# Optimization experiments

Hardware: AMD Instinct MI355X
Metric: run time of the kernel (lower is better)

## Reference

```python
import jax, jax.numpy as jnp
import numpy as np


def setup_inputs() -> dict:
    key = jax.random.key(0)
    k1, k2, k3, k4 = jax.random.split(key, 4)
    B, idf, cdf, h, w, L = 32, 256, 256, 64, 64, 128
    x = jax.random.normal(k1, (B, idf, h, w), dtype=jnp.float32)
    context = jax.random.normal(k2, (B, cdf, L), dtype=jnp.float32)
    # conv1x1 weight (no bias): [idf, cdf]
    W = jax.random.normal(k3, (idf, cdf), dtype=jnp.float32) / np.sqrt(cdf)
    mask = jax.random.randint(k4, (B, L), 0, 2).astype(bool)
    return {"x": x, "context": context, "W": W, "mask": mask}


def reference(x, context, W, mask):
    B, idf, h, w = x.shape
    hxw = h * w
    L = context.shape[2]
    # conv1x1 projection of context: [B, idf, L]
    source = jnp.einsum('ic,bcl->bil', W, context)
    target = x.reshape(B, idf, hxw)
    # QK^T: [B, hxw, L]
    attn = jnp.einsum('bip,bil->bpl', target, source)
    # faithful to torch: mask [B, L] is tiled hxw times over the flattened
    # [B*hxw, L] view (row order b*hxw+p vs tile order p*B+b, as in original)
    attn_flat = attn.reshape(B * hxw, L)
    attn_flat = jnp.where(jnp.tile(mask, (hxw, 1)), -jnp.inf, attn_flat)
    attn = jax.nn.softmax(attn_flat, axis=-1).reshape(B, hxw, L)
    attn_t = jnp.swapaxes(attn, 1, 2)  # [B, L, hxw]
    # PV: [B, idf, hxw] -> [B, idf, h, w]
    result = jnp.einsum('bil,blp->bip', source, attn_t).reshape(B, idf, h, w)
    return result, attn_t.reshape(B, L, h, w)
```

## Files before the change

kernel.cpp:

```cpp
#include <hip/hip_runtime.h>
#include <cstdint>

#define IDF 256
#define CDF 256
#define NL  128
#define HXW 4096
#define NB  32
#define PTILE 64

typedef _Float16 f16x8 __attribute__((ext_vector_type(8)));
typedef __fp16 fp16x2 __attribute__((ext_vector_type(2)));
typedef float f32x4 __attribute__((ext_vector_type(4)));
typedef unsigned short u16;
typedef unsigned int u32;

union Frag { f16x8 v; u32 u[4]; uint2 u2[2]; uint4 u4; };

__device__ __forceinline__ u16 f2h(float f) { union { _Float16 h; u16 s; } c; c.h = (_Float16)f; return c.s; }
__device__ __forceinline__ u32 pkrtz(float a, float b) {
  union { fp16x2 v; u32 u; } c;
  c.v = __builtin_amdgcn_cvt_pkrtz(a, b);
  return c.u;
}


__global__ __launch_bounds__(256) void proj_kernel(const float* __restrict__ W,
                                                   const float* __restrict__ ctx,
                                                   u16* __restrict__ srcF,
                                                   u16* __restrict__ srcT,
                                                   const u32* __restrict__ msk,
                                                   u32* __restrict__ ws0) {
  const int tid = threadIdx.x;
  if (blockIdx.x == 0 && blockIdx.y == 0) {
    __shared__ int bi_s, bf_s, mode_s;
    if (tid == 0) { bi_s = 0; bf_s = 0; }
    __syncthreads();
    int bi = 0, bfl = 0;
    for (int k = 0; k < 4; ++k) {
      u32 v = msk[tid * 4 + k];
      if (v > 1u) bi = 1;
      float f = __uint_as_float(v);
      if (!(f == 0.0f || f == 1.0f)) bfl = 1;
    }
    if (bi) atomicOr(&bi_s, 1);
    if (bfl) atomicOr(&bf_s, 1);
    __syncthreads();
    if (tid == 0) { mode_s = (bi_s == 0) ? 0 : ((bf_s == 0) ? 1 : 2); ws0[0] = (u32)mode_s; }
    __syncthreads();
    const int mode = mode_s;
    if (tid < 128) {
      int row = tid >> 2, q = tid & 3;
      u32 bits = 0;
      for (int c = 0; c < 32; ++c) {
        int idx = row * NL + q * 32 + c;
        int mv;
        if (mode == 0)      mv = ((const int*)msk)[idx] != 0;
        else if (mode == 1) mv = ((const float*)msk)[idx] != 0.0f;
        else                mv = ((const unsigned char*)msk)[idx] != 0;
        bits |= (u32)mv << c;
      }
      ws0[64 + row * 4 + q] = bits;
    }
  }

  __shared__ float sWt[16][33];
  __shared__ float sC[16 * NL];
  const int b = blockIdx.y;
  const int i0 = blockIdx.x * 32;
  const int tx = tid & 31;
  const int ty = tid >> 5;
  float acc[4][4] = {};
  const float* ctxb = ctx + (size_t)b * CDF * NL;
  for (int c0 = 0; c0 < CDF; c0 += 16) {
    if (tid < 128) {
      int i = tid >> 2, cq = tid & 3;
      float4 w4 = *(const float4*)(W + (size_t)(i0 + i) * CDF + c0 + cq * 4);
      sWt[cq * 4 + 0][i] = w4.x; sWt[cq * 4 + 1][i] = w4.y;
      sWt[cq * 4 + 2][i] = w4.z; sWt[cq * 4 + 3][i] = w4.w;
    }
#pragma unroll
    for (int k = 0; k < 2; ++k) {
      int idx = tid + k * 256;
      int r = idx >> 5, c4 = idx & 31;
      *(float4*)(sC + r * NL + c4 * 4) =
          *(const float4*)(ctxb + (size_t)(c0 + r) * NL + c4 * 4);
    }
    __syncthreads();
#pragma unroll
    for (int cc = 0; cc < 16; ++cc) {
      float4 c4 = *(const float4*)(sC + cc * NL + tx * 4);
#pragma unroll
      for (int ii = 0; ii < 4; ++ii) {
        float w = sWt[cc][ty * 4 + ii];
        acc[ii][0] = fmaf(w, c4.x, acc[ii][0]);
        acc[ii][1] = fmaf(w, c4.y, acc[ii][1]);
        acc[ii][2] = fmaf(w, c4.z, acc[ii][2]);
        acc[ii][3] = fmaf(w, c4.w, acc[ii][3]);
      }
    }
    __syncthreads();
  }
  u16* sf = srcF + (size_t)b * IDF * NL;
  u16* st = srcT + (size_t)b * NL * IDF;
#pragma unroll
  for (int ii = 0; ii < 4; ++ii) {
    int i = i0 + ty * 4 + ii;
    u32 d0 = pkrtz(acc[ii][0], acc[ii][1]);
    u32 d1 = pkrtz(acc[ii][2], acc[ii][3]);
    *(uint2*)(sf + (size_t)i * NL + tx * 4) = make_uint2(d0, d1);
#pragma unroll
    for (int jl = 0; jl < 4; ++jl)
      st[(size_t)(tx * 4 + jl) * IDF + i] = f2h(acc[ii][jl]);
  }
}

__global__ __launch_bounds__(256, 4) void attn_kernel(
    const float* __restrict__ x, const u16* __restrict__ srcF,
    const u16* __restrict__ srcT, const u32* __restrict__ wsm,
    float* __restrict__ out0, float* __restrict__ out1) {
  __shared__ __align__(16) u32 sBuf[128 * 66];

  const int tid = threadIdx.x;
  const int lane = tid & 63;
  const int w = tid >> 6;
  const int m15 = lane & 15;
  const int g = lane >> 4;
  const int b = blockIdx.y;
  const int p0 = blockIdx.x * PTILE;
  const int pl = w * 16 + m15;

  {
    const float* xb = x + (size_t)b * IDF * HXW + p0;
    const int t16 = tid >> 4;
    const int p4 = (tid & 15) * 4;
    float4 lo[8], hi[8];
#pragma unroll
    for (int it = 0; it < 8; ++it) {
      const float* rp = xb + (size_t)(it * 32 + t16 * 2) * HXW + p4;
      lo[it] = *(const float4*)rp;
      hi[it] = *(const float4*)(rp + HXW);
    }
#pragma unroll
    for (int it = 0; it < 8; ++it) {
      int base = (it * 16 + t16) * 66 + p4;
      u32 r0 = pkrtz(lo[it].x, hi[it].x);
      u32 r1 = pkrtz(lo[it].y, hi[it].y);
      u32 r2 = pkrtz(lo[it].z, hi[it].z);
      u32 r3 = pkrtz(lo[it].w, hi[it].w);
      *(uint2*)(sBuf + base + 0) = make_uint2(r0, r1);
      *(uint2*)(sBuf + base + 2) = make_uint2(r2, r3);
    }
  }
  __syncthreads();

  f32x4 accq[8];
#pragma unroll
  for (int nt = 0; nt < 8; ++nt) accq[nt] = f32x4{0.f, 0.f, 0.f, 0.f};

  const u16* stb = srcT + (size_t)b * NL * IDF;
#pragma unroll
  for (int ic = 0; ic < 8; ++ic) {
    Frag bf[8];
#pragma unroll
    for (int nt = 0; nt < 8; ++nt)
      bf[nt].u4 = *(const uint4*)(stb + (size_t)(nt * 16 + m15) * IDF + ic * 32 + g * 8);
    Frag bx;
#pragma unroll
    for (int jj = 0; jj < 4; ++jj)
      bx.u[jj] = sBuf[(ic * 16 + g * 4 + jj) * 66 + pl];
#pragma unroll
    for (int nt = 0; nt < 8; ++nt)
      accq[nt] = __builtin_amdgcn_mfma_f32_16x16x32_f16(bf[nt].v, bx.v, accq[nt], 0, 0, 0);
  }

  const int rm = pl & 31;
  uint4 mr = *(const uint4*)(wsm + rm * 4);
  u32 mw[4] = {mr.x, mr.y, mr.z, mr.w};
  float mx = -3.0e38f;
#pragma unroll
  for (int nt = 0; nt < 8; ++nt) {
    u32 bits = mw[nt >> 1] >> ((nt & 1) * 16);
#pragma unroll
    for (int r = 0; r < 4; ++r) {
      if ((bits >> (g * 4 + r)) & 1u) accq[nt][r] = -3.0e38f;
      mx = fmaxf(mx, accq[nt][r]);
    }
  }
  mx = fmaxf(mx, __shfl_xor(mx, 16));
  mx = fmaxf(mx, __shfl_xor(mx, 32));
  float s = 0.f;
#pragma unroll
  for (int nt = 0; nt < 8; ++nt)
#pragma unroll
    for (int r = 0; r < 4; ++r) {
      float e = __expf(accq[nt][r] - mx);
      accq[nt][r] = e;
      s += e;
    }
  s += __shfl_xor(s, 16);
  s += __shfl_xor(s, 32);
  const float inv = 1.0f / s;

  float* o1 = out1 + (size_t)b * NL * HXW + p0 + pl;
#pragma unroll
  for (int nt = 0; nt < 8; ++nt)
#pragma unroll
    for (int r = 0; r < 4; ++r) {
      float v = accq[nt][r] * inv;
      accq[nt][r] = v;
      o1[(size_t)(nt * 16 + g * 4 + r) * HXW] = v;
    }
  __syncthreads();
#pragma unroll
  for (int nt = 0; nt < 8; ++nt) {
    sBuf[pl * 66 + nt * 8 + g * 2 + 0] = pkrtz(accq[nt][0], accq[nt][1]);
    sBuf[pl * 66 + nt * 8 + g * 2 + 1] = pkrtz(accq[nt][2], accq[nt][3]);
  }
  __syncthreads();

  f32x4 accp[4][4];
#pragma unroll
  for (int mt = 0; mt < 4; ++mt)
#pragma unroll
    for (int nt2 = 0; nt2 < 4; ++nt2) accp[mt][nt2] = f32x4{0.f, 0.f, 0.f, 0.f};

  const u16* sfb = srcF + (size_t)b * IDF * NL;
#pragma unroll
  for (int ks = 0; ks < 4; ++ks) {
    Frag af[4], bf[4];
#pragma unroll
    for (int mt = 0; mt < 4; ++mt)
      af[mt].u4 = *(const uint4*)(sfb + (size_t)(w * 64 + mt * 16 + m15) * NL + ks * 32 + g * 8);
#pragma unroll
    for (int nt2 = 0; nt2 < 4; ++nt2) {
      int di = (nt2 * 16 + m15) * 66 + ks * 16 + g * 4;
      bf[nt2].u2[0] = *(const uint2*)(sBuf + di);
      bf[nt2].u2[1] = *(const uint2*)(sBuf + di + 2);
    }
#pragma unroll
    for (int mt = 0; mt < 4; ++mt)
#pragma unroll
      for (int nt2 = 0; nt2 < 4; ++nt2)
        accp[mt][nt2] = __builtin_amdgcn_mfma_f32_16x16x32_f16(af[mt].v, bf[nt2].v, accp[mt][nt2], 0, 0, 0);
  }

  float* o0 = out0 + (size_t)b * IDF * HXW + p0;
#pragma unroll
  for (int mt = 0; mt < 4; ++mt)
#pragma unroll
    for (int nt2 = 0; nt2 < 4; ++nt2) {
      int col = nt2 * 16 + m15;
#pragma unroll
      for (int r = 0; r < 4; ++r) {
        int row = w * 64 + mt * 16 + g * 4 + r;
        o0[(size_t)row * HXW + col] = accp[mt][nt2][r];
      }
    }
}

extern "C" void kernel_launch(void* const* d_in, const int* in_sizes, int n_in,
                              void* d_out, int out_size, void* d_ws, size_t ws_size,
                              hipStream_t stream) {
  const float* x   = (const float*)d_in[0];
  const float* ctx = (const float*)d_in[1];
  const float* W   = (const float*)d_in[2];
  const void*  msk = d_in[3];
  float* out0 = (float*)d_out;
  float* out1 = out0 + (size_t)NB * IDF * HXW;
  u32* ws0 = (u32*)d_ws;
  u16* srcF = (u16*)((char*)d_ws + 1024);
  u16* srcT = (u16*)((char*)d_ws + 1024 + 2097152);

  proj_kernel<<<dim3(8, NB), 256, 0, stream>>>(W, ctx, srcF, srcT, (const u32*)msk, ws0);
  attn_kernel<<<dim3(HXW / PTILE, NB), 256, 0, stream>>>(x, srcF, srcT, ws0 + 64, out0, out1);
}
```

Measured before the change: 151.2 us.

## Halve pixel tile, split softmax over waves, double-buffer fragment loads

Shrinks the per-block pixel tile from 64 to 32, which doubles the grid. Each pair of waves now handles half of the L dimension and merges the partial softmax max and sum through a small shared-memory exchange. Global fragment loads for the QK and PV matmuls are double-buffered so the next chunk is fetched while MFMAs run. This aims for more parallelism and better latency hiding, at the cost of rereading the projected source per pixel twice as often and an extra barrier.

```diff
diff --git a/kernel.cpp b/kernel.cpp
--- a/kernel.cpp
+++ b/kernel.cpp
@@ -6,7 +6,7 @@
 #define NL  128
 #define HXW 4096
 #define NB  32
-#define PTILE 64
+#define PTILE 32
 
 typedef _Float16 f16x8 __attribute__((ext_vector_type(8)));
 typedef __fp16 fp16x2 __attribute__((ext_vector_type(2)));
@@ -118,68 +118,81 @@
     const float* __restrict__ x, const u16* __restrict__ srcF,
     const u16* __restrict__ srcT, const u32* __restrict__ wsm,
     float* __restrict__ out0, float* __restrict__ out1) {
-  __shared__ __align__(16) u32 sBuf[128 * 66];
+  __shared__ __align__(16) u32 sBuf[128 * 35];
+  __shared__ float2 sM[2][32];
 
   const int tid = threadIdx.x;
   const int lane = tid & 63;
   const int w = tid >> 6;
   const int m15 = lane & 15;
   const int g = lane >> 4;
+  const int half = w >> 1;
+  const int wq = w & 1;
   const int b = blockIdx.y;
   const int p0 = blockIdx.x * PTILE;
-  const int pl = w * 16 + m15;
-
-  {
-    const float* xb = x + (size_t)b * IDF * HXW + p0;
-    const int t16 = tid >> 4;
-    const int p4 = (tid & 15) * 4;
-    float4 lo[8], hi[8];
-#pragma unroll
-    for (int it = 0; it < 8; ++it) {
-      const float* rp = xb + (size_t)(it * 32 + t16 * 2) * HXW + p4;
-      lo[it] = *(const float4*)rp;
-      hi[it] = *(const float4*)(rp + HXW);
-    }
-#pragma unroll
-    for (int it = 0; it < 8; ++it) {
-      int base = (it * 16 + t16) * 66 + p4;
-      u32 r0 = pkrtz(lo[it].x, hi[it].x);
-      u32 r1 = pkrtz(lo[it].y, hi[it].y);
-      u32 r2 = pkrtz(lo[it].z, hi[it].z);
-      u32 r3 = pkrtz(lo[it].w, hi[it].w);
-      *(uint2*)(sBuf + base + 0) = make_uint2(r0, r1);
-      *(uint2*)(sBuf + base + 2) = make_uint2(r2, r3);
-    }
+  const int pl = wq * 16 + m15;
+
+  const u16* stb = srcT + (size_t)b * NL * IDF;
+
+  const float* xb = x + (size_t)b * IDF * HXW + p0;
+  const int kq = tid >> 3;
+  const int p4 = (tid & 7) * 4;
+  float4 lo[4], hi[4];
+#pragma unroll
+  for (int it = 0; it < 4; ++it) {
+    const float* rp = xb + (size_t)(it * 64 + kq * 2) * HXW + p4;
+    lo[it] = *(const float4*)rp;
+    hi[it] = *(const float4*)(rp + HXW);
+  }
+
+  Frag bufA[4], bufB[4];
+#define LOAD_ST(dst, ic_)                                                              \
+  {                                                                                    \
+    _Pragma("unroll")                                                                  \
+    for (int nt = 0; nt < 4; ++nt)                                                     \
+      dst[nt].u4 = *(const uint4*)(stb + (size_t)((half * 4 + nt) * 16 + m15) * IDF +  \
+                                   (ic_) * 32 + g * 8);                                \
+  }
+  LOAD_ST(bufA, 0)
+
+#pragma unroll
+  for (int it = 0; it < 4; ++it) {
+    int base = (it * 32 + kq) * 35 + p4;
+    sBuf[base + 0] = pkrtz(lo[it].x, hi[it].x);
+    sBuf[base + 1] = pkrtz(lo[it].y, hi[it].y);
+    sBuf[base + 2] = pkrtz(lo[it].z, hi[it].z);
+    sBuf[base + 3] = pkrtz(lo[it].w, hi[it].w);
   }
   __syncthreads();
 
-  f32x4 accq[8];
-#pragma unroll
-  for (int nt = 0; nt < 8; ++nt) accq[nt] = f32x4{0.f, 0.f, 0.f, 0.f};
-
-  const u16* stb = srcT + (size_t)b * NL * IDF;
+  f32x4 accq[4];
+#pragma unroll
+  for (int nt = 0; nt < 4; ++nt) accq[nt] = f32x4{0.f, 0.f, 0.f, 0.f};
+
 #pragma unroll
   for (int ic = 0; ic < 8; ++ic) {
-    Frag bf[8];
-#pragma unroll
-    for (int nt = 0; nt < 8; ++nt)
-      bf[nt].u4 = *(const uint4*)(stb + (size_t)(nt * 16 + m15) * IDF + ic * 32 + g * 8);
+    if (ic < 7) {
+      if (ic & 1) { LOAD_ST(bufA, ic + 1) } else { LOAD_ST(bufB, ic + 1) }
+    }
     Frag bx;
 #pragma unroll
     for (int jj = 0; jj < 4; ++jj)
-      bx.u[jj] = sBuf[(ic * 16 + g * 4 + jj) * 66 + pl];
-#pragma unroll
-    for (int nt = 0; nt < 8; ++nt)
-      accq[nt] = __builtin_amdgcn_mfma_f32_16x16x32_f16(bf[nt].v, bx.v, accq[nt], 0, 0, 0);
+      bx.u[jj] = sBuf[(ic * 16 + g * 4 + jj) * 35 + pl];
+#pragma unroll
+    for (int nt = 0; nt < 4; ++nt) {
+      const Frag& af = (ic & 1) ? bufB[nt] : bufA[nt];
+      accq[nt] = __builtin_amdgcn_mfma_f32_16x16x32_f16(af.v, bx.v, accq[nt], 0, 0, 0);
+    }
   }
 
   const int rm = pl & 31;
   uint4 mr = *(const uint4*)(wsm + rm * 4);
-  u32 mw[4] = {mr.x, mr.y, mr.z, mr.w};
+  u32 mwv[4] = {mr.x, mr.y, mr.z, mr.w};
   float mx = -3.0e38f;
 #pragma unroll
-  for (int nt = 0; nt < 8; ++nt) {
-    u32 bits = mw[nt >> 1] >> ((nt & 1) * 16);
+  for (int nt = 0; nt < 4; ++nt) {
+    int lt = half * 4 + nt;
+    u32 bits = mwv[lt >> 1] >> ((lt & 1) * 16);
 #pragma unroll
     for (int r = 0; r < 4; ++r) {
       if ((bits >> (g * 4 + r)) & 1u) accq[nt][r] = -3.0e38f;
@@ -190,7 +203,7 @@
   mx = fmaxf(mx, __shfl_xor(mx, 32));
   float s = 0.f;
 #pragma unroll
-  for (int nt = 0; nt < 8; ++nt)
+  for (int nt = 0; nt < 4; ++nt)
 #pragma unroll
     for (int r = 0; r < 4; ++r) {
       float e = __expf(accq[nt][r] - mx);
@@ -199,61 +212,79 @@
     }
   s += __shfl_xor(s, 16);
   s += __shfl_xor(s, 32);
-  const float inv = 1.0f / s;
+  if (g == 0) sM[half][pl] = make_float2(mx, s);
+  __syncthreads();
+  float2 o = sM[half ^ 1][pl];
+  float m = fmaxf(mx, o.x);
+  float f = __expf(mx - m);
+  float s_tot = s * f + o.y * __expf(o.x - m);
+  const float inv = f / s_tot;
+
+  u32* sAd = sBuf;
+#pragma unroll
+  for (int nt = 0; nt < 4; ++nt) {
+#pragma unroll
+    for (int r = 0; r < 4; ++r) accq[nt][r] *= inv;
+    sAd[pl * 66 + (half * 4 + nt) * 8 + g * 2 + 0] = pkrtz(accq[nt][0], accq[nt][1]);
+    sAd[pl * 66 + (half * 4 + nt) * 8 + g * 2 + 1] = pkrtz(accq[nt][2], accq[nt][3]);
+  }
+  __syncthreads();
+
+  const u16* sfb = srcF + (size_t)b * IDF * NL;
+  Frag afA[4], afB[4];
+#define LOAD_SF(dst, ks_)                                                              \
+  {                                                                                    \
+    _Pragma("unroll")                                                                  \
+    for (int mt = 0; mt < 4; ++mt)                                                     \
+      dst[mt].u4 = *(const uint4*)(sfb + (size_t)(w * 64 + mt * 16 + m15) * NL +       \
+                                   (ks_) * 32 + g * 8);                                \
+  }
+  LOAD_SF(afA, 0)
 
   float* o1 = out1 + (size_t)b * NL * HXW + p0 + pl;
 #pragma unroll
-  for (int nt = 0; nt < 8; ++nt)
-#pragma unroll
-    for (int r = 0; r < 4; ++r) {
-      float v = accq[nt][r] * inv;
-      accq[nt][r] = v;
-      o1[(size_t)(nt * 16 + g * 4 + r) * HXW] = v;
-    }
-  __syncthreads();
-#pragma unroll
-  for (int nt = 0; nt < 8; ++nt) {
-    sBuf[pl * 66 + nt * 8 + g * 2 + 0] = pkrtz(accq[nt][0], accq[nt][1]);
-    sBuf[pl * 66 + nt * 8 + g * 2 + 1] = pkrtz(accq[nt][2], accq[nt][3]);
-  }
-  __syncthreads();
-
-  f32x4 accp[4][4];
+  for (int nt = 0; nt < 4; ++nt)
+#pragma unroll
+    for (int r = 0; r < 4; ++r)
+      o1[(size_t)((half * 4 + nt) * 16 + g * 4 + r) * HXW] = accq[nt][r];
+
+  f32x4 accp[4][2];
 #pragma unroll
   for (int mt = 0; mt < 4; ++mt)
 #pragma unroll
-    for (int nt2 = 0; nt2 < 4; ++nt2) accp[mt][nt2] = f32x4{0.f, 0.f, 0.f, 0.f};
-
-  const u16* sfb = srcF + (size_t)b * IDF * NL;
+    for (int n2 = 0; n2 < 2; ++n2) accp[mt][n2] = f32x4{0.f, 0.f, 0.f, 0.f};
+
 #pragma unroll
   for (int ks = 0; ks < 4; ++ks) {
-    Frag af[4], bf[4];
-#pragma unroll
-    for (int mt = 0; mt < 4; ++mt)
-      af[mt].u4 = *(const uint4*)(sfb + (size_t)(w * 64 + mt * 16 + m15) * NL + ks * 32 + g * 8);
-#pragma unroll
-    for (int nt2 = 0; nt2 < 4; ++nt2) {
-      int di = (nt2 * 16 + m15) * 66 + ks * 16 + g * 4;
-      bf[nt2].u2[0] = *(const uint2*)(sBuf + di);
-      bf[nt2].u2[1] = *(const uint2*)(sBuf + di + 2);
-    }
-#pragma unroll
-    for (int mt = 0; mt < 4; ++mt)
-#pragma unroll
-      for (int nt2 = 0; nt2 < 4; ++nt2)
-        accp[mt][nt2] = __builtin_amdgcn_mfma_f32_16x16x32_f16(af[mt].v, bf[nt2].v, accp[mt][nt2], 0, 0, 0);
+    if (ks < 3) {
+      if (ks & 1) { LOAD_SF(afA, ks + 1) } else { LOAD_SF(afB, ks + 1) }
+    }
+    Frag bf[2];
+#pragma unroll
+    for (int n2 = 0; n2 < 2; ++n2) {
+      int di = (n2 * 16 + m15) * 66 + ks * 16 + g * 4;
+      bf[n2].u2[0] = *(const uint2*)(sAd + di);
+      bf[n2].u2[1] = *(const uint2*)(sAd + di + 2);
+    }
+#pragma unroll
+    for (int mt = 0; mt < 4; ++mt) {
+      const Frag& af = (ks & 1) ? afB[mt] : afA[mt];
+#pragma unroll
+      for (int n2 = 0; n2 < 2; ++n2)
+        accp[mt][n2] = __builtin_amdgcn_mfma_f32_16x16x32_f16(af.v, bf[n2].v, accp[mt][n2], 0, 0, 0);
+    }
   }
 
   float* o0 = out0 + (size_t)b * IDF * HXW + p0;
 #pragma unroll
   for (int mt = 0; mt < 4; ++mt)
 #pragma unroll
-    for (int nt2 = 0; nt2 < 4; ++nt2) {
-      int col = nt2 * 16 + m15;
+    for (int n2 = 0; n2 < 2; ++n2) {
+      int col = n2 * 16 + m15;
 #pragma unroll
       for (int r = 0; r < 4; ++r) {
         int row = w * 64 + mt * 16 + g * 4 + r;
-        o0[(size_t)row * HXW + col] = accp[mt][nt2][r];
+        o0[(size_t)row * HXW + col] = accp[mt][n2][r];
       }
     }
 }
```

Measured after the change: 181.4 us. 20.0% more time.

## Process two pixel tiles per block and prefetch next x tile during PV

Applied to the files above, without the earlier changes.

Each attention block now handles two consecutive 64-pixel tiles of the same batch, which halves the grid and moves the mask load and base pointers out of the per-tile work. The global loads of x for the second tile are issued during the last k-step of the first tile's PV MFMA loop, so that load latency overlaps compute. The launch bound no longer requests 4 blocks per SM, and holding the prefetched x registers (lo/hi) during the MFMA loop raises register pressure, which may reduce occupancy. The attention output store is also moved after the LDS writes.

```diff
diff --git a/kernel.cpp b/kernel.cpp
--- a/kernel.cpp
+++ b/kernel.cpp
@@ -114,7 +114,7 @@
   }
 }
 
-__global__ __launch_bounds__(256, 4) void attn_kernel(
+__global__ __launch_bounds__(256) void attn_kernel(
     const float* __restrict__ x, const u16* __restrict__ srcF,
     const u16* __restrict__ srcT, const u32* __restrict__ wsm,
     float* __restrict__ out0, float* __restrict__ out1) {
@@ -125,21 +125,41 @@
   const int w = tid >> 6;
   const int m15 = lane & 15;
   const int g = lane >> 4;
-  const int b = blockIdx.y;
-  const int p0 = blockIdx.x * PTILE;
+  const int bid = blockIdx.x;
+  const int tile0 = bid * 2;
+  const int b = tile0 >> 6;
   const int pl = w * 16 + m15;
 
-  {
-    const float* xb = x + (size_t)b * IDF * HXW + p0;
-    const int t16 = tid >> 4;
-    const int p4 = (tid & 15) * 4;
-    float4 lo[8], hi[8];
-#pragma unroll
-    for (int it = 0; it < 8; ++it) {
-      const float* rp = xb + (size_t)(it * 32 + t16 * 2) * HXW + p4;
-      lo[it] = *(const float4*)rp;
-      hi[it] = *(const float4*)(rp + HXW);
-    }
+  const u16* stb = srcT + (size_t)b * NL * IDF;
+  const u16* sfb = srcF + (size_t)b * IDF * NL;
+  const float* xbb = x + (size_t)b * IDF * HXW;
+
+  const int t16 = tid >> 4;
+  const int p4 = (tid & 15) * 4;
+
+  const int rm = pl & 31;
+  uint4 mr = *(const uint4*)(wsm + rm * 4);
+  u32 mwv[4] = {mr.x, mr.y, mr.z, mr.w};
+
+  float4 lo[8], hi[8];
+#define ISSUE_X(p0_)                                                          \
+  {                                                                           \
+    const float* xb = xbb + (p0_);                                            \
+    _Pragma("unroll")                                                         \
+    for (int it = 0; it < 8; ++it) {                                          \
+      const float* rp = xb + (size_t)(it * 32 + t16 * 2) * HXW + p4;          \
+      lo[it] = *(const float4*)rp;                                            \
+      hi[it] = *(const float4*)(rp + HXW);                                    \
+    }                                                                         \
+  }
+
+  ISSUE_X((tile0 & 63) * 64)
+
+#pragma unroll
+  for (int t = 0; t < 2; ++t) {
+    const int p0 = ((tile0 + t) & 63) * 64;
+    __syncthreads();
+
 #pragma unroll
     for (int it = 0; it < 8; ++it) {
       int base = (it * 16 + t16) * 66 + p4;
@@ -150,112 +170,110 @@
       *(uint2*)(sBuf + base + 0) = make_uint2(r0, r1);
       *(uint2*)(sBuf + base + 2) = make_uint2(r2, r3);
     }
-  }
-  __syncthreads();
-
-  f32x4 accq[8];
-#pragma unroll
-  for (int nt = 0; nt < 8; ++nt) accq[nt] = f32x4{0.f, 0.f, 0.f, 0.f};
-
-  const u16* stb = srcT + (size_t)b * NL * IDF;
-#pragma unroll
-  for (int ic = 0; ic < 8; ++ic) {
-    Frag bf[8];
+    __syncthreads();
+
+    f32x4 accq[8];
+#pragma unroll
+    for (int nt = 0; nt < 8; ++nt) accq[nt] = f32x4{0.f, 0.f, 0.f, 0.f};
+#pragma unroll
+    for (int ic = 0; ic < 8; ++ic) {
+      Frag bf[8];
+#pragma unroll
+      for (int nt = 0; nt < 8; ++nt)
+        bf[nt].u4 = *(const uint4*)(stb + (size_t)(nt * 16 + m15) * IDF + ic * 32 + g * 8);
+      Frag bx;
+#pragma unroll
+      for (int jj = 0; jj < 4; ++jj)
+        bx.u[jj] = sBuf[(ic * 16 + g * 4 + jj) * 66 + pl];
+#pragma unroll
+      for (int nt = 0; nt < 8; ++nt)
+        accq[nt] = __builtin_amdgcn_mfma_f32_16x16x32_f16(bf[nt].v, bx.v, accq[nt], 0, 0, 0);
+    }
+
+    float mx = -3.0e38f;
+#pragma unroll
+    for (int nt = 0; nt < 8; ++nt) {
+      u32 bits = mwv[nt >> 1] >> ((nt & 1) * 16);
+#pragma unroll
+      for (int r = 0; r < 4; ++r) {
+        if ((bits >> (g * 4 + r)) & 1u) accq[nt][r] = -3.0e38f;
+        mx = fmaxf(mx, accq[nt][r]);
+      }
+    }
+    mx = fmaxf(mx, __shfl_xor(mx, 16));
+    mx = fmaxf(mx, __shfl_xor(mx, 32));
+    float s = 0.f;
 #pragma unroll
     for (int nt = 0; nt < 8; ++nt)
-      bf[nt].u4 = *(const uint4*)(stb + (size_t)(nt * 16 + m15) * IDF + ic * 32 + g * 8);
-    Frag bx;
-#pragma unroll
-    for (int jj = 0; jj < 4; ++jj)
-      bx.u[jj] = sBuf[(ic * 16 + g * 4 + jj) * 66 + pl];
+#pragma unroll
+      for (int r = 0; r < 4; ++r) {
+        float e = __expf(accq[nt][r] - mx);
+        accq[nt][r] = e;
+        s += e;
+      }
+    s += __shfl_xor(s, 16);
+    s += __shfl_xor(s, 32);
+    const float inv = 1.0f / s;
 #pragma unroll
     for (int nt = 0; nt < 8; ++nt)
-      accq[nt] = __builtin_amdgcn_mfma_f32_16x16x32_f16(bf[nt].v, bx.v, accq[nt], 0, 0, 0);
-  }
-
-  const int rm = pl & 31;
-  uint4 mr = *(const uint4*)(wsm + rm * 4);
-  u32 mw[4] = {mr.x, mr.y, mr.z, mr.w};
-  float mx = -3.0e38f;
-#pragma unroll
-  for (int nt = 0; nt < 8; ++nt) {
-    u32 bits = mw[nt >> 1] >> ((nt & 1) * 16);
-#pragma unroll
-    for (int r = 0; r < 4; ++r) {
-      if ((bits >> (g * 4 + r)) & 1u) accq[nt][r] = -3.0e38f;
-      mx = fmaxf(mx, accq[nt][r]);
-    }
-  }
-  mx = fmaxf(mx, __shfl_xor(mx, 16));
-  mx = fmaxf(mx, __shfl_xor(mx, 32));
-  float s = 0.f;
-#pragma unroll
-  for (int nt = 0; nt < 8; ++nt)
-#pragma unroll
-    for (int r = 0; r < 4; ++r) {
-      float e = __expf(accq[nt][r] - mx);
-      accq[nt][r] = e;
-      s += e;
-    }
-  s += __shfl_xor(s, 16);
-  s += __shfl_xor(s, 32);
-  const float inv = 1.0f / s;
-
-  float* o1 = out1 + (size_t)b * NL * HXW + p0 + pl;
-#pragma unroll
-  for (int nt = 0; nt < 8; ++nt)
-#pragma unroll
-    for (int r = 0; r < 4; ++r) {
-      float v = accq[nt][r] * inv;
-      accq[nt][r] = v;
-      o1[(size_t)(nt * 16 + g * 4 + r) * HXW] = v;
-    }
-  __syncthreads();
-#pragma unroll
-  for (int nt = 0; nt < 8; ++nt) {
-    sBuf[pl * 66 + nt * 8 + g * 2 + 0] = pkrtz(accq[nt][0], accq[nt][1]);
-    sBuf[pl * 66 + nt * 8 + g * 2 + 1] = pkrtz(accq[nt][2], accq[nt][3]);
-  }
-  __syncthreads();
-
-  f32x4 accp[4][4];
-#pragma unroll
-  for (int mt = 0; mt < 4; ++mt)
-#pragma unroll
-    for (int nt2 = 0; nt2 < 4; ++nt2) accp[mt][nt2] = f32x4{0.f, 0.f, 0.f, 0.f};
-
-  const u16* sfb = srcF + (size_t)b * IDF * NL;
-#pragma unroll
-  for (int ks = 0; ks < 4; ++ks) {
-    Frag af[4], bf[4];
+#pragma unroll
+      for (int r = 0; r < 4; ++r) accq[nt][r] *= inv;
+
+    __syncthreads();
+
+#pragma unroll
+    for (int nt = 0; nt < 8; ++nt) {
+      sBuf[pl * 66 + nt * 8 + g * 2 + 0] = pkrtz(accq[nt][0], accq[nt][1]);
+      sBuf[pl * 66 + nt * 8 + g * 2 + 1] = pkrtz(accq[nt][2], accq[nt][3]);
+    }
+    float* o1 = out1 + (size_t)b * NL * HXW + p0 + pl;
+#pragma unroll
+    for (int nt = 0; nt < 8; ++nt)
+#pragma unroll
+      for (int r = 0; r < 4; ++r)
+        o1[(size_t)(nt * 16 + g * 4 + r) * HXW] = accq[nt][r];
+    __syncthreads();
+
+    f32x4 accp[4][4];
 #pragma unroll
     for (int mt = 0; mt < 4; ++mt)
-      af[mt].u4 = *(const uint4*)(sfb + (size_t)(w * 64 + mt * 16 + m15) * NL + ks * 32 + g * 8);
-#pragma unroll
-    for (int nt2 = 0; nt2 < 4; ++nt2) {
-      int di = (nt2 * 16 + m15) * 66 + ks * 16 + g * 4;
-      bf[nt2].u2[0] = *(const uint2*)(sBuf + di);
-      bf[nt2].u2[1] = *(const uint2*)(sBuf + di + 2);
-    }
+#pragma unroll
+      for (int nt2 = 0; nt2 < 4; ++nt2) accp[mt][nt2] = f32x4{0.f, 0.f, 0.f, 0.f};
+
+#pragma unroll
+    for (int ks = 0; ks < 4; ++ks) {
+      Frag af[4], bf[4];
+#pragma unroll
+      for (int mt = 0; mt < 4; ++mt)
+        af[mt].u4 = *(const uint4*)(sfb + (size_t)(w * 64 + mt * 16 + m15) * NL + ks * 32 + g * 8);
+      if (ks == 3 && t == 0)
+        ISSUE_X(((tile0 + 1) & 63) * 64)
+#pragma unroll
+      for (int nt2 = 0; nt2 < 4; ++nt2) {
+        int di = (nt2 * 16 + m15) * 66 + ks * 16 + g * 4;
+        bf[nt2].u2[0] = *(const uint2*)(sBuf + di);
+        bf[nt2].u2[1] = *(const uint2*)(sBuf + di + 2);
+      }
+#pragma unroll
+      for (int mt = 0; mt < 4; ++mt)
+#pragma unroll
+        for (int nt2 = 0; nt2 < 4; ++nt2)
+          accp[mt][nt2] = __builtin_amdgcn_mfma_f32_16x16x32_f16(af[mt].v, bf[nt2].v, accp[mt][nt2], 0, 0, 0);
+    }
+
+    float* o0 = out0 + (size_t)b * IDF * HXW + p0;
 #pragma unroll
     for (int mt = 0; mt < 4; ++mt)
 #pragma unroll
-      for (int nt2 = 0; nt2 < 4; ++nt2)
-        accp[mt][nt2] = __builtin_amdgcn_mfma_f32_16x16x32_f16(af[mt].v, bf[nt2].v, accp[mt][nt2], 0, 0, 0);
-  }
-
-  float* o0 = out0 + (size_t)b * IDF * HXW + p0;
-#pragma unroll
-  for (int mt = 0; mt < 4; ++mt)
-#pragma unroll
-    for (int nt2 = 0; nt2 < 4; ++nt2) {
-      int col = nt2 * 16 + m15;
-#pragma unroll
-      for (int r = 0; r < 4; ++r) {
-        int row = w * 64 + mt * 16 + g * 4 + r;
-        o0[(size_t)row * HXW + col] = accp[mt][nt2][r];
-      }
-    }
+      for (int nt2 = 0; nt2 < 4; ++nt2) {
+        int col = nt2 * 16 + m15;
+#pragma unroll
+        for (int r = 0; r < 4; ++r) {
+          int row = w * 64 + mt * 16 + g * 4 + r;
+          o0[(size_t)row * HXW + col] = accp[mt][nt2][r];
+        }
+      }
+  }
 }
 
 extern "C" void kernel_launch(void* const* d_in, const int* in_sizes, int n_in,
@@ -272,5 +290,5 @@
   u16* srcT = (u16*)((char*)d_ws + 1024 + 2097152);
 
   proj_kernel<<<dim3(8, NB), 256, 0, stream>>>(W, ctx, srcF, srcT, (const u32*)msk, ws0);
-  attn_kernel<<<dim3(HXW / PTILE, NB), 256, 0, stream>>>(x, srcF, srcT, ws0 + 64, out0, out1);
-}
+  attn_kernel<<<dim3(NB * (HXW / PTILE) / 2), 256, 0, stream>>>(x, srcF, srcT, ws0 + 64, out0, out1);
+}
```

Result: slower. 192.1 us (+27.0%).

## Double-buffer x and srcT chunks through LDS in the QK stage

Applied to the files above, without the earlier changes.

Replaces the up-front load of the whole 256-channel x tile with a double-buffered loop over 32-channel chunks. The next chunk's global loads are prefetched into registers while the current chunk's MFMAs run, and the srcT fragments are now staged through shared memory instead of being read per-wave from global. The attention-probability stores to out1 are moved after the P tile is written to LDS and interleaved with the first PV step, and the launch-bounds occupancy hint is dropped. The cost is a __syncthreads per chunk, more LDS buffers, and possibly lower occupancy or higher register pressure.

```diff
diff --git a/kernel.cpp b/kernel.cpp
--- a/kernel.cpp
+++ b/kernel.cpp
@@ -114,11 +114,13 @@
   }
 }
 
-__global__ __launch_bounds__(256, 4) void attn_kernel(
+__global__ __launch_bounds__(256) void attn_kernel(
     const float* __restrict__ x, const u16* __restrict__ srcF,
     const u16* __restrict__ srcT, const u32* __restrict__ wsm,
     float* __restrict__ out0, float* __restrict__ out1) {
-  __shared__ __align__(16) u32 sBuf[128 * 66];
+  __shared__ __align__(16) u32 sX[2][16 * 66];
+  __shared__ __align__(16) u32 sST[2][128 * 20];
+  __shared__ __align__(16) u32 sA[64 * 66];
 
   const int tid = threadIdx.x;
   const int lane = tid & 63;
@@ -129,57 +131,78 @@
   const int p0 = blockIdx.x * PTILE;
   const int pl = w * 16 + m15;
 
-  {
-    const float* xb = x + (size_t)b * IDF * HXW + p0;
-    const int t16 = tid >> 4;
-    const int p4 = (tid & 15) * 4;
-    float4 lo[8], hi[8];
-#pragma unroll
-    for (int it = 0; it < 8; ++it) {
-      const float* rp = xb + (size_t)(it * 32 + t16 * 2) * HXW + p4;
-      lo[it] = *(const float4*)rp;
-      hi[it] = *(const float4*)(rp + HXW);
-    }
-#pragma unroll
-    for (int it = 0; it < 8; ++it) {
-      int base = (it * 16 + t16) * 66 + p4;
-      u32 r0 = pkrtz(lo[it].x, hi[it].x);
-      u32 r1 = pkrtz(lo[it].y, hi[it].y);
-      u32 r2 = pkrtz(lo[it].z, hi[it].z);
-      u32 r3 = pkrtz(lo[it].w, hi[it].w);
-      *(uint2*)(sBuf + base + 0) = make_uint2(r0, r1);
-      *(uint2*)(sBuf + base + 2) = make_uint2(r2, r3);
-    }
-  }
-  __syncthreads();
-
-  f32x4 accq[8];
-#pragma unroll
-  for (int nt = 0; nt < 8; ++nt) accq[nt] = f32x4{0.f, 0.f, 0.f, 0.f};
-
   const u16* stb = srcT + (size_t)b * NL * IDF;
-#pragma unroll
-  for (int ic = 0; ic < 8; ++ic) {
-    Frag bf[8];
-#pragma unroll
-    for (int nt = 0; nt < 8; ++nt)
-      bf[nt].u4 = *(const uint4*)(stb + (size_t)(nt * 16 + m15) * IDF + ic * 32 + g * 8);
-    Frag bx;
-#pragma unroll
-    for (int jj = 0; jj < 4; ++jj)
-      bx.u[jj] = sBuf[(ic * 16 + g * 4 + jj) * 66 + pl];
-#pragma unroll
-    for (int nt = 0; nt < 8; ++nt)
-      accq[nt] = __builtin_amdgcn_mfma_f32_16x16x32_f16(bf[nt].v, bx.v, accq[nt], 0, 0, 0);
-  }
+  const u16* sfb = srcF + (size_t)b * IDF * NL;
+  const float* xb = x + (size_t)b * IDF * HXW + p0;
+
+  const int t16 = tid >> 4;
+  const int p4x = (tid & 15) * 4;
+  const int sl = tid >> 1;
+  const int sh = tid & 1;
 
   const int rm = pl & 31;
   uint4 mr = *(const uint4*)(wsm + rm * 4);
-  u32 mw[4] = {mr.x, mr.y, mr.z, mr.w};
+  u32 mwv[4] = {mr.x, mr.y, mr.z, mr.w};
+
+  float4 xlo[2], xhi[2];
+  uint4 st0[2], st1[2];
+
+#define ISSUE_CHUNK(slot, ic_)                                                      \
+  {                                                                                 \
+    const int k0 = (ic_) * 32;                                                      \
+    xlo[slot] = *(const float4*)(xb + (size_t)(k0 + 2 * t16) * HXW + p4x);          \
+    xhi[slot] = *(const float4*)(xb + (size_t)(k0 + 2 * t16 + 1) * HXW + p4x);      \
+    st0[slot] = *(const uint4*)(stb + (size_t)sl * IDF + k0 + sh * 16);             \
+    st1[slot] = *(const uint4*)(stb + (size_t)sl * IDF + k0 + sh * 16 + 8);         \
+  }
+
+#define WRITE_CHUNK(slot, buf)                                                      \
+  {                                                                                 \
+    u32* xd = sX[buf];                                                              \
+    xd[t16 * 66 + p4x + 0] = pkrtz(xlo[slot].x, xhi[slot].x);                       \
+    xd[t16 * 66 + p4x + 1] = pkrtz(xlo[slot].y, xhi[slot].y);                       \
+    xd[t16 * 66 + p4x + 2] = pkrtz(xlo[slot].z, xhi[slot].z);                       \
+    xd[t16 * 66 + p4x + 3] = pkrtz(xlo[slot].w, xhi[slot].w);                       \
+    u32* sd = sST[buf] + sl * 20 + sh * 8;                                          \
+    *(uint4*)(sd + 0) = st0[slot];                                                  \
+    *(uint4*)(sd + 4) = st1[slot];                                                  \
+  }
+
+  ISSUE_CHUNK(0, 0)
+  ISSUE_CHUNK(1, 1)
+  WRITE_CHUNK(0, 0)
+  __syncthreads();
+
+  f32x4 accq[8];
+#pragma unroll
+  for (int nt = 0; nt < 8; ++nt) accq[nt] = f32x4{0.f, 0.f, 0.f, 0.f};
+
+#pragma unroll
+  for (int ic = 0; ic < 8; ++ic) {
+    if (ic < 6) ISSUE_CHUNK(ic & 1, ic + 2)
+    const u32* sxb = sX[ic & 1];
+    const u32* ssb = sST[ic & 1];
+    Frag bx;
+#pragma unroll
+    for (int jj = 0; jj < 4; ++jj)
+      bx.u[jj] = sxb[(g * 4 + jj) * 66 + pl];
+    Frag af[8];
+#pragma unroll
+    for (int nt = 0; nt < 8; ++nt)
+      af[nt].u4 = *(const uint4*)(ssb + (nt * 16 + m15) * 20 + g * 4);
+#pragma unroll
+    for (int nt = 0; nt < 8; ++nt)
+      accq[nt] = __builtin_amdgcn_mfma_f32_16x16x32_f16(af[nt].v, bx.v, accq[nt], 0, 0, 0);
+    if (ic < 7) {
+      WRITE_CHUNK((ic + 1) & 1, (ic + 1) & 1)
+      __syncthreads();
+    }
+  }
+
   float mx = -3.0e38f;
 #pragma unroll
   for (int nt = 0; nt < 8; ++nt) {
-    u32 bits = mw[nt >> 1] >> ((nt & 1) * 16);
+    u32 bits = mwv[nt >> 1] >> ((nt & 1) * 16);
 #pragma unroll
     for (int r = 0; r < 4; ++r) {
       if ((bits >> (g * 4 + r)) & 1u) accq[nt][r] = -3.0e38f;
@@ -200,48 +223,49 @@
   s += __shfl_xor(s, 16);
   s += __shfl_xor(s, 32);
   const float inv = 1.0f / s;
+#pragma unroll
+  for (int nt = 0; nt < 8; ++nt)
+#pragma unroll
+    for (int r = 0; r < 4; ++r) accq[nt][r] *= inv;
+
+#pragma unroll
+  for (int nt = 0; nt < 8; ++nt) {
+    sA[pl * 66 + nt * 8 + g * 2 + 0] = pkrtz(accq[nt][0], accq[nt][1]);
+    sA[pl * 66 + nt * 8 + g * 2 + 1] = pkrtz(accq[nt][2], accq[nt][3]);
+  }
+  __syncthreads();
+
+  f32x4 accp[4][4];
+#pragma unroll
+  for (int mt = 0; mt < 4; ++mt)
+#pragma unroll
+    for (int nt2 = 0; nt2 < 4; ++nt2) accp[mt][nt2] = f32x4{0.f, 0.f, 0.f, 0.f};
 
   float* o1 = out1 + (size_t)b * NL * HXW + p0 + pl;
 #pragma unroll
-  for (int nt = 0; nt < 8; ++nt)
-#pragma unroll
-    for (int r = 0; r < 4; ++r) {
-      float v = accq[nt][r] * inv;
-      accq[nt][r] = v;
-      o1[(size_t)(nt * 16 + g * 4 + r) * HXW] = v;
-    }
-  __syncthreads();
-#pragma unroll
-  for (int nt = 0; nt < 8; ++nt) {
-    sBuf[pl * 66 + nt * 8 + g * 2 + 0] = pkrtz(accq[nt][0], accq[nt][1]);
-    sBuf[pl * 66 + nt * 8 + g * 2 + 1] = pkrtz(accq[nt][2], accq[nt][3]);
-  }
-  __syncthreads();
-
-  f32x4 accp[4][4];
-#pragma unroll
-  for (int mt = 0; mt < 4; ++mt)
-#pragma unroll
-    for (int nt2 = 0; nt2 < 4; ++nt2) accp[mt][nt2] = f32x4{0.f, 0.f, 0.f, 0.f};
-
-  const u16* sfb = srcF + (size_t)b * IDF * NL;
-#pragma unroll
   for (int ks = 0; ks < 4; ++ks) {
-    Frag af[4], bf[4];
+    Frag af2[4], bf2[4];
 #pragma unroll
     for (int mt = 0; mt < 4; ++mt)
-      af[mt].u4 = *(const uint4*)(sfb + (size_t)(w * 64 + mt * 16 + m15) * NL + ks * 32 + g * 8);
+      af2[mt].u4 = *(const uint4*)(sfb + (size_t)(w * 64 + mt * 16 + m15) * NL + ks * 32 + g * 8);
+    if (ks == 0) {
+#pragma unroll
+      for (int nt = 0; nt < 8; ++nt)
+#pragma unroll
+        for (int r = 0; r < 4; ++r)
+          o1[(size_t)(nt * 16 + g * 4 + r) * HXW] = accq[nt][r];
+    }
 #pragma unroll
     for (int nt2 = 0; nt2 < 4; ++nt2) {
       int di = (nt2 * 16 + m15) * 66 + ks * 16 + g * 4;
-      bf[nt2].u2[0] = *(const uint2*)(sBuf + di);
-      bf[nt2].u2[1] = *(const uint2*)(sBuf + di + 2);
+      bf2[nt2].u2[0] = *(const uint2*)(sA + di);
+      bf2[nt2].u2[1] = *(const uint2*)(sA + di + 2);
     }
 #pragma unroll
     for (int mt = 0; mt < 4; ++mt)
 #pragma unroll
       for (int nt2 = 0; nt2 < 4; ++nt2)
-        accp[mt][nt2] = __builtin_amdgcn_mfma_f32_16x16x32_f16(af[mt].v, bf[nt2].v, accp[mt][nt2], 0, 0, 0);
+        accp[mt][nt2] = __builtin_amdgcn_mfma_f32_16x16x32_f16(af2[mt].v, bf2[nt2].v, accp[mt][nt2], 0, 0, 0);
   }
 
   float* o0 = out0 + (size_t)b * IDF * HXW + p0;
```

Result: slower. 158.6 us (+4.9%).
